# Kernel optimization log

Measured on AMD Instinct MI355X. Metric: run time of the kernel, lower is better.

## Reference

```python
import jax, jax.numpy as jnp
import numpy as np

NUM_NODES, NODE_F = 50000, 128
NUM_EDGES, EDGE_F = 500000, 128
B, N = 4096, 100
D = 64      # node_dim
T = 8       # time_dim
LN_EPS = 1e-5


def setup_inputs() -> dict:
    key = jax.random.key(0)
    ks = jax.random.split(key, 16)
    inp = {
        'src_neighbor_node_ids': jax.random.randint(ks[0], (B, N), 0, NUM_NODES),
        'src_neighbor_edge_ids': jax.random.randint(ks[1], (B, N), 0, NUM_EDGES),
        'src_neighbor_times': jax.random.uniform(ks[2], (B, N), dtype=jnp.float32),
        'dst_node_ids': jax.random.randint(ks[3], (B,), 0, NUM_NODES),
        'node_raw_features': jax.random.normal(ks[4], (NUM_NODES, NODE_F), jnp.float32),
        'edge_raw_features': jax.random.normal(ks[5], (NUM_EDGES, EDGE_F), jnp.float32),
        # projection layers (stored as [in, out])
        'W_feat': jax.random.normal(ks[6], (NODE_F, D), jnp.float32) / np.sqrt(NODE_F),
        'b_feat': jnp.zeros((D,), jnp.float32),
        'W_edge': jax.random.normal(ks[7], (1, D), jnp.float32),
        'b_edge': jnp.zeros((D,), jnp.float32),
        'W_time': jax.random.normal(ks[8], (T, D), jnp.float32) / np.sqrt(T),
        'b_time': jnp.zeros((D,), jnp.float32),
        'W_struct': jax.random.normal(ks[9], (1, D), jnp.float32),
        'b_struct': jnp.zeros((D,), jnp.float32),
        # time encoder (cosine basis with log-spaced frequencies)
        'w_tenc': (1.0 / 10 ** np.linspace(0, 9, T)).astype(np.float32),
        'b_tenc': jnp.zeros((T,), jnp.float32),
        # layernorm
        'ln_g': jnp.ones((D,), jnp.float32),
        'ln_b': jnp.zeros((D,), jnp.float32),
        # GCNConv
        'W_gcn': jax.random.normal(ks[10], (D, D), jnp.float32) / np.sqrt(D),
        'b_gcn': jnp.zeros((D,), jnp.float32),
        # output layer
        'W_out': jax.random.normal(ks[11], (D, D), jnp.float32) / np.sqrt(D),
        'b_out': jnp.zeros((D,), jnp.float32),
    }
    return inp


def reference(src_neighbor_node_ids, src_neighbor_edge_ids, src_neighbor_times,
              dst_node_ids, node_raw_features, edge_raw_features,
              W_feat, b_feat, W_edge, b_edge, W_time, b_time, W_struct, b_struct,
              w_tenc, b_tenc, ln_g, ln_b, W_gcn, b_gcn, W_out, b_out):
    f32 = jnp.float32
    nbr_raw = node_raw_features[src_neighbor_node_ids]            # [B,N,F]
    node_f = nbr_raw @ W_feat + b_feat                            # [B,N,D]
    edge_col = edge_raw_features[src_neighbor_edge_ids, 0][..., None]  # [B,N,1]
    edge_f = edge_col @ W_edge + b_edge
    t_enc = jnp.cos(src_neighbor_times[..., None] * w_tenc + b_tenc)   # [B,N,T]
    time_f = t_enc @ W_time + b_time
    co = (src_neighbor_node_ids == dst_node_ids[:, None]).astype(f32)[..., None]
    co_f = co @ W_struct + b_struct
    skill_nbr = nbr_raw[..., 0].astype(jnp.int32)                 # [B,N]
    skill_dst = node_raw_features[dst_node_ids, 0].astype(jnp.int32)  # [B]
    sim = (skill_nbr == skill_dst[:, None]).astype(f32)[..., None]
    sim_f = sim @ W_struct + b_struct
    fused = node_f + edge_f + time_f + co_f + sim_f               # [B,N,D]
    mu = fused.mean(-1, keepdims=True)
    var = ((fused - mu) ** 2).mean(-1, keepdims=True)
    fused = (fused - mu) * jax.lax.rsqrt(var + LN_EPS) * ln_g + ln_b
    # per-sample chain GCN: directed edges j -> j+1 for j in [0, v-2], v = #valid ids,
    # PyG gcn_norm with self loops: deg[j] = 1 + in_degree[j]
    h = fused @ W_gcn                                             # [B,N,D]
    v = (src_neighbor_node_ids > 0).sum(-1)                       # [B]
    pos = jnp.arange(N)[None, :]                                  # [1,N]
    has_in = ((pos >= 1) & (pos < v[:, None])).astype(f32)        # [B,N]
    deg = 1.0 + has_in
    dinv_sqrt = jax.lax.rsqrt(deg)
    h_prev = jnp.pad(h[:, :-1], ((0, 0), (1, 0), (0, 0)))
    d_prev = jnp.pad(dinv_sqrt[:, :-1], ((0, 0), (1, 0)))
    out = h / deg[..., None] + (has_in * d_prev * dinv_sqrt)[..., None] * h_prev + b_gcn
    gnn = jax.nn.relu(out)
    src_emb = gnn.mean(axis=1)                                    # [B,D] global_mean_pool over N
    dst_emb = node_raw_features[dst_node_ids] @ W_feat + b_feat
    src_emb = src_emb @ W_out + b_out
    dst_emb = dst_emb @ W_out + b_out
    return src_emb, dst_emb
```

## Files before the change

kernel.cpp:

```cpp
#include <hip/hip_runtime.h>
#include <stdint.h>

#define NUM_NODES 50000
#define B_ 4096
#define N_ 100

typedef float f32x4 __attribute__((ext_vector_type(4)));
typedef float f32x2 __attribute__((ext_vector_type(2)));
typedef int   i32x4 __attribute__((ext_vector_type(4)));
typedef short s16x8 __attribute__((ext_vector_type(8)));

__device__ inline unsigned short f2bf(float f) {
    unsigned u = __float_as_uint(f);
    u += 0x7fffu + ((u >> 16) & 1u);
    return (unsigned short)(u >> 16);
}

template <int CTRL>
__device__ inline float dpp_add(float x) {
    int t = __builtin_amdgcn_update_dpp(0, __float_as_int(x), CTRL, 0xf, 0xf, true);
    return x + __int_as_float(t);
}
__device__ inline float wave_sum64(float x) {
    x = dpp_add<0x111>(x);
    x = dpp_add<0x112>(x);
    x = dpp_add<0x114>(x);
    x = dpp_add<0x118>(x);
    x = dpp_add<0x142>(x);
    x = dpp_add<0x143>(x);
    return __int_as_float(__builtin_amdgcn_readlane(__float_as_int(x), 63));
}

__global__ __launch_bounds__(256) void k_pre(
    const float* __restrict__ node_raw, const float* __restrict__ W_feat,
    const float* __restrict__ b_feat, const float* __restrict__ W_gcn,
    const float* __restrict__ ln_g, const float* __restrict__ ln_b,
    const float* __restrict__ W_edge, const float* __restrict__ b_edge,
    const float* __restrict__ W_time, const float* __restrict__ b_time,
    const float* __restrict__ W_struct, const float* __restrict__ b_struct,
    float* __restrict__ proj, int* __restrict__ skill,
    float* __restrict__ hb, float* __restrict__ wmg, float* __restrict__ Mg,
    unsigned short* __restrict__ PGmF)
{
    __shared__ float red[4][64];
    __shared__ float PGms[12][64];
    __shared__ unsigned short WfB[16][64][8];
    int blk = blockIdx.x;
    int t = threadIdx.x;
    int dj = t & 63;

    if (blk == gridDim.x - 1) {
        int g = t >> 6;
        float acc = 0.f;
        #pragma unroll
        for (int i = 0; i < 16; ++i) {
            int dk = g * 16 + i;
            acc += ln_b[dk] * W_gcn[dk * 64 + dj];
        }
        red[g][dj] = acc;

        if (t < 64) {
            int d = t;
            float col[11];
            col[0] = W_edge[d];
            col[1] = W_struct[d];
            #pragma unroll
            for (int i = 0; i < 8; ++i) col[2 + i] = W_time[i * 64 + d];
            col[10] = b_edge[d] + b_time[d] + 2.f * b_struct[d];
            float wmv[11];
            #pragma unroll
            for (int j = 0; j < 11; ++j) wmv[j] = wave_sum64(col[j]) * (1.f / 64.f);
            float cc[11];
            #pragma unroll
            for (int j = 0; j < 11; ++j) cc[j] = col[j] - wmv[j];
            #pragma unroll
            for (int j = 0; j < 11; ++j) {
                #pragma unroll
                for (int k = j; k < 11; ++k) {
                    float m = wave_sum64(cc[j] * cc[k]);
                    if (t == 0) { Mg[j * 11 + k] = m; Mg[k * 11 + j] = m; }
                }
            }
            if (t == 0) {
                #pragma unroll
                for (int j = 0; j < 11; ++j) wmg[j] = wmv[j];
            }

            int j = t;
            float accp[12];
            #pragma unroll
            for (int m = 0; m < 12; ++m) accp[m] = 0.f;
            for (int d2 = 0; d2 < 64; ++d2) {
                float gg = ln_g[d2] * W_gcn[d2 * 64 + j];
                float bias_d = b_edge[d2] + b_time[d2] + 2.f * b_struct[d2];
                accp[0] = fmaf(W_edge[d2], gg, accp[0]);
                accp[1] = fmaf(W_struct[d2], gg, accp[1]);
                #pragma unroll
                for (int i = 0; i < 8; ++i)
                    accp[2 + i] = fmaf(W_time[i * 64 + d2], gg, accp[2 + i]);
                accp[10] = fmaf(bias_d, gg, accp[10]);
                accp[11] += gg;
            }
            #pragma unroll
            for (int m = 0; m < 12; ++m) PGms[m][j] = accp[m];
        }
        __syncthreads();
        if (g == 0) hb[dj] = red[0][dj] + red[1][dj] + red[2][dj] + red[3][dj];

        {
            int ct = t >> 6, l = t & 63;
            int col = ct * 16 + (l & 15);
            int ks = (l >> 4) * 8;
            s16x8 a2;
            #pragma unroll
            for (int j2 = 0; j2 < 8; ++j2) {
                int k = ks + j2;
                a2[j2] = (k < 12) ? (short)f2bf(PGms[k][col]) : (short)0;
            }
            *(s16x8*)(PGmF + ((size_t)ct * 64 + l) * 8) = a2;
        }
        return;
    }

    #pragma unroll
    for (int i = 0; i < 4; ++i) {
        int e = t + i * 256;
        int tile = e >> 6;
        int l = e & 63;
        int ct = tile >> 2, kt = tile & 3;
        int col = ct * 16 + (l & 15);
        int ks = kt * 32 + (l >> 4) * 8;
        s16x8 a;
        #pragma unroll
        for (int j = 0; j < 8; ++j)
            a[j] = (short)f2bf(W_feat[(ks + j) * 64 + col]);
        *(s16x8*)&WfB[tile][l][0] = a;
    }
    __syncthreads();

    int w = t >> 6, lane = t & 63;
    int rbase = blk * 64 + w * 16;
    int rA = rbase + (lane & 15);
    int rc = rA < NUM_NODES ? rA : (NUM_NODES - 1);
    int kq = lane >> 4;

    s16x8 A[4];
    float a0x = 0.f;
    #pragma unroll
    for (int kt = 0; kt < 4; ++kt) {
        const float* src = node_raw + (size_t)rc * 128 + kt * 32 + kq * 8;
        f32x4 v0 = *(const f32x4*)src;
        f32x4 v1 = *(const f32x4*)(src + 4);
        s16x8 a;
        a[0] = (short)f2bf(v0.x); a[1] = (short)f2bf(v0.y);
        a[2] = (short)f2bf(v0.z); a[3] = (short)f2bf(v0.w);
        a[4] = (short)f2bf(v1.x); a[5] = (short)f2bf(v1.y);
        a[6] = (short)f2bf(v1.z); a[7] = (short)f2bf(v1.w);
        A[kt] = a;
        if (kt == 0) a0x = v0.x;
    }
    if (kq == 0 && rA < NUM_NODES) skill[rA] = (int)a0x;

    f32x4 acc[4];
    #pragma unroll
    for (int ct = 0; ct < 4; ++ct) { f32x4 z = {0.f,0.f,0.f,0.f}; acc[ct] = z; }
    #pragma unroll
    for (int ct = 0; ct < 4; ++ct) {
        #pragma unroll
        for (int kt = 0; kt < 4; ++kt) {
            s16x8 bfr = *(const s16x8*)&WfB[ct * 4 + kt][lane][0];
            acc[ct] = __builtin_amdgcn_mfma_f32_16x16x32_bf16(A[kt], bfr, acc[ct], 0, 0, 0);
        }
    }
    #pragma unroll
    for (int ct = 0; ct < 4; ++ct) {
        int col = ct * 16 + (lane & 15);
        float bf = b_feat[col];
        #pragma unroll
        for (int j = 0; j < 4; ++j) {
            int row = rbase + kq * 4 + j;
            if (row < NUM_NODES)
                proj[(size_t)row * 64 + col] = acc[ct][j] + bf;
        }
    }
}

__global__ __launch_bounds__(256) void k_pg(
    const float* __restrict__ proj, const float* __restrict__ W_gcn,
    const float* __restrict__ ln_g,
    const float* __restrict__ W_out, const float* __restrict__ b_out,
    const float* __restrict__ W_edge, const float* __restrict__ b_edge,
    const float* __restrict__ W_time, const float* __restrict__ b_time,
    const float* __restrict__ W_struct, const float* __restrict__ b_struct,
    float* __restrict__ projG, float* __restrict__ dstE,
    float* __restrict__ stats)
{
    __shared__ unsigned short WgB[8][64][8];
    __shared__ unsigned short WoB[8][64][8];
    __shared__ unsigned short WsB[2][64][8];
    int t = threadIdx.x;

    #pragma unroll
    for (int i = 0; i < 2; ++i) {
        int e = t + i * 256;
        int tile = e >> 6, l = e & 63;
        int ct = tile >> 1, kt = tile & 1;
        int col = ct * 16 + (l & 15);
        int ks = kt * 32 + (l >> 4) * 8;
        s16x8 a, b2;
        #pragma unroll
        for (int j = 0; j < 8; ++j) {
            int k = ks + j;
            a[j]  = (short)f2bf(ln_g[k] * W_gcn[k * 64 + col]);
            b2[j] = (short)f2bf(W_out[k * 64 + col]);
        }
        *(s16x8*)&WgB[tile][l][0] = a;
        *(s16x8*)&WoB[tile][l][0] = b2;
    }
    if (t < 128) {
        int kt = t >> 6, l = t & 63;
        int col = l & 15;
        int ks = kt * 32 + (l >> 4) * 8;
        s16x8 a;
        #pragma unroll
        for (int j = 0; j < 8; ++j) {
            int d = ks + j;
            float v;
            if (col == 0) v = W_edge[d];
            else if (col == 1) v = W_struct[d];
            else if (col < 10) v = W_time[(col - 2) * 64 + d];
            else if (col == 10) v = b_edge[d] + b_time[d] + 2.f * b_struct[d];
            else if (col == 11) v = 1.f;
            else v = 0.f;
            a[j] = (short)f2bf(v);
        }
        *(s16x8*)&WsB[kt][l][0] = a;
    }
    __syncthreads();

    int w = t >> 6, lane = t & 63;
    int rbase = blockIdx.x * 64 + w * 16;
    int rA = rbase + (lane & 15);
    int rc = rA < NUM_NODES ? rA : (NUM_NODES - 1);
    int kq = lane >> 4;

    s16x8 Ahi[2], Alo[2], Qhi[2], Qlo[2];
    #pragma unroll
    for (int kt = 0; kt < 2; ++kt) {
        const float* src = proj + (size_t)rc * 64 + kt * 32 + kq * 8;
        f32x4 v0 = *(const f32x4*)src;
        f32x4 v1 = *(const f32x4*)(src + 4);
        #pragma unroll
        for (int j = 0; j < 8; ++j) {
            float v = (j < 4) ? v0[j] : v1[j - 4];
            unsigned short hi = f2bf(v);
            float rem = v - __uint_as_float((unsigned)hi << 16);
            Ahi[kt][j] = (short)hi;
            Alo[kt][j] = (short)f2bf(rem);
            float p2 = v * v;
            unsigned short h2 = f2bf(p2);
            float r2 = p2 - __uint_as_float((unsigned)h2 << 16);
            Qhi[kt][j] = (short)h2;
            Qlo[kt][j] = (short)f2bf(r2);
        }
    }

    f32x4 accG[4], accE[4];
    f32x4 accS = {0.f, 0.f, 0.f, 0.f}, accQ = {0.f, 0.f, 0.f, 0.f};
    #pragma unroll
    for (int ct = 0; ct < 4; ++ct) {
        f32x4 z = {0.f, 0.f, 0.f, 0.f};
        accG[ct] = z; accE[ct] = z;
    }
    #pragma unroll
    for (int ct = 0; ct < 4; ++ct) {
        #pragma unroll
        for (int kt = 0; kt < 2; ++kt) {
            s16x8 bg = *(const s16x8*)&WgB[ct * 2 + kt][lane][0];
            accG[ct] = __builtin_amdgcn_mfma_f32_16x16x32_bf16(Alo[kt], bg, accG[ct], 0, 0, 0);
            accG[ct] = __builtin_amdgcn_mfma_f32_16x16x32_bf16(Ahi[kt], bg, accG[ct], 0, 0, 0);
            s16x8 bo = *(const s16x8*)&WoB[ct * 2 + kt][lane][0];
            accE[ct] = __builtin_amdgcn_mfma_f32_16x16x32_bf16(Alo[kt], bo, accE[ct], 0, 0, 0);
            accE[ct] = __builtin_amdgcn_mfma_f32_16x16x32_bf16(Ahi[kt], bo, accE[ct], 0, 0, 0);
        }
    }
    #pragma unroll
    for (int kt = 0; kt < 2; ++kt) {
        s16x8 bs = *(const s16x8*)&WsB[kt][lane][0];
        accS = __builtin_amdgcn_mfma_f32_16x16x32_bf16(Alo[kt], bs, accS, 0, 0, 0);
        accS = __builtin_amdgcn_mfma_f32_16x16x32_bf16(Ahi[kt], bs, accS, 0, 0, 0);
        accQ = __builtin_amdgcn_mfma_f32_16x16x32_bf16(Qlo[kt], bs, accQ, 0, 0, 0);
        accQ = __builtin_amdgcn_mfma_f32_16x16x32_bf16(Qhi[kt], bs, accQ, 0, 0, 0);
    }

    #pragma unroll
    for (int ct = 0; ct < 4; ++ct) {
        int col = ct * 16 + (lane & 15);
        float bo_ = b_out[col];
        #pragma unroll
        for (int j = 0; j < 4; ++j) {
            int row = rbase + kq * 4 + j;
            if (row < NUM_NODES) {
                projG[(size_t)row * 64 + col] = accG[ct][j];
                dstE[(size_t)row * 64 + col] = accE[ct][j] + bo_;
            }
        }
    }
    int c = lane & 15;
    if (c <= 11) {
        #pragma unroll
        for (int j = 0; j < 4; ++j) {
            int row = rbase + kq * 4 + j;
            if (row < NUM_NODES) stats[(size_t)row * 16 + c] = accS[j];
        }
    }
    if (c == 11) {
        #pragma unroll
        for (int j = 0; j < 4; ++j) {
            int row = rbase + kq * 4 + j;
            if (row < NUM_NODES) stats[(size_t)row * 16 + 12] = accQ[j];
        }
    }
}

__global__ __launch_bounds__(256) void k_main(
    const int* __restrict__ ids, const int* __restrict__ eids,
    const float* __restrict__ times, const int* __restrict__ dst_ids,
    const float* __restrict__ edge_raw,
    const float* __restrict__ w_tenc, const float* __restrict__ b_tenc,
    const float* __restrict__ b_gcn, const float* __restrict__ W_out,
    const float* __restrict__ b_out,
    const float* __restrict__ projG, const float* __restrict__ dstE,
    const int* __restrict__ skill,
    const float* __restrict__ hb, const float* __restrict__ wmg,
    const float* __restrict__ Mg, const unsigned short* __restrict__ PGmF,
    const float* __restrict__ stats,
    float* __restrict__ out)
{
    __shared__ int ids_s[112];
    __shared__ unsigned short VA[112 * 32];
    __shared__ float rstd_s[112];
    __shared__ f32x2 cf_s[112];
    __shared__ float pooled[64];
    __shared__ int vcnt_w[4];

    int b = blockIdx.x;
    int t = threadIdx.x;
    int lane = t & 63, w = t >> 6;

    int dstb = dst_ids[b];
    int skdst = skill[dstb];

    int idx_c = t < N_ ? t : 0;
    int id_t = ids[b * N_ + idx_c];
    float tm_t = times[b * N_ + idx_c];
    int ei_t = eids[b * N_ + idx_c];
    if (t < 112) ids_s[t] = (t < N_) ? id_t : 0;
    unsigned long long bal = __ballot((t < N_) && (id_t > 0));
    if (lane == 0) vcnt_w[w] = __popcll(bal);
    float tc[8];
    #pragma unroll
    for (int i = 0; i < 8; ++i) tc[i] = __cosf(fmaf(tm_t, w_tenc[i], b_tenc[i]));
    __syncthreads();
    int v = vcnt_w[0] + vcnt_w[1] + vcnt_w[2] + vcnt_w[3];

    int colw = 16 * w + (lane & 15);
    int kq = lane >> 4;
    float pgv[7][4];
    #pragma unroll
    for (int mt = 0; mt < 7; ++mt) {
        i32x4 s4 = *(const i32x4*)&ids_s[mt * 16 + kq * 4];
        #pragma unroll
        for (int j = 0; j < 4; ++j)
            pgv[mt][j] = projG[(size_t)s4[j] * 64 + colw];
    }
    if (w == 3)
        out[(size_t)(B_ + b) * 64 + lane] = dstE[(size_t)dstb * 64 + lane];

    if (t < 112) {
        int n = t;
        bool hin = (n >= 1) && (n < v);
        float a_ = hin ? 0.5f : 1.f;
        float dprev = (n >= 2 && n <= v) ? 0.70710678118f : 1.f;
        float coef = hin ? dprev * 0.70710678118f : 0.f;
        f32x2 cf = {a_, coef};
        cf_s[t] = cf;
    }

    if (t < N_) {
        float e_t = edge_raw[(size_t)ei_t * 128];
        int sk_t = skill[id_t];
        const f32x4* sp4 = (const f32x4*)(stats + (size_t)id_t * 16);
        f32x4 s0 = sp4[0], s1 = sp4[1], s2 = sp4[2];
        float spp = stats[(size_t)id_t * 16 + 12];

        float u[11];
        u[0] = e_t;
        u[1] = (id_t == dstb ? 1.f : 0.f) + (sk_t == skdst ? 1.f : 0.f);
        #pragma unroll
        for (int i = 0; i < 8; ++i) u[2 + i] = tc[i];
        u[10] = 1.f;

        float pwv[11] = {s0.x, s0.y, s0.z, s0.w, s1.x, s1.y, s1.z, s1.w,
                         s2.x, s2.y, s2.z};
        float sp = s2.w;
        float dot_upw = 0.f, su_wm = 0.f;
        #pragma unroll
        for (int j = 0; j < 11; ++j) {
            dot_upw = fmaf(u[j], pwv[j], dot_upw);
            su_wm = fmaf(u[j], wmg[j], su_wm);
        }
        float mu = sp * (1.f / 64.f) + su_wm;
        float q = spp + sp * sp * (1.f / 64.f) + 2.f * dot_upw - 2.f * sp * mu;
        #pragma unroll
        for (int j = 0; j < 11; ++j) {
            float tj = 0.f;
            #pragma unroll
            for (int k = 0; k < 11; ++k) tj = fmaf(Mg[j * 11 + k], u[k], tj);
            q = fmaf(u[j], tj, q);
        }
        float rstd = rsqrtf(fmaxf(q, 0.f) * (1.f / 64.f) + 1e-5f);
        rstd_s[t] = rstd;

        unsigned short vv[32];
        #pragma unroll
        for (int j = 0; j < 11; ++j) vv[j] = f2bf(rstd * u[j]);
        vv[11] = f2bf(-rstd * mu);
        #pragma unroll
        for (int j = 12; j < 32; ++j) vv[j] = 0;
        #pragma unroll
        for (int c = 0; c < 4; ++c)
            *(s16x8*)((char*)VA + t * 64 + ((c ^ (t & 3)) * 16)) = *(const s16x8*)&vv[c * 8];
    } else if (t < 112) {
        rstd_s[t] = 0.f;
        s16x8 z = {0, 0, 0, 0, 0, 0, 0, 0};
        #pragma unroll
        for (int c = 0; c < 4; ++c)
            *(s16x8*)((char*)VA + t * 64 + c * 16) = z;
    }
    __syncthreads();

    s16x8 bfr = *(const s16x8*)(PGmF + ((size_t)w * 64 + lane) * 8);
    f32x4 acc[7];
    #pragma unroll
    for (int mt = 0; mt < 7; ++mt) {
        int row = mt * 16 + (lane & 15);
        s16x8 a = *(const s16x8*)((char*)VA + row * 64 + ((kq ^ (row & 3)) * 16));
        f32x4 z = {0.f, 0.f, 0.f, 0.f};
        acc[mt] = __builtin_amdgcn_mfma_f32_16x16x32_bf16(a, bfr, z, 0, 0, 0);
    }

    float hbv = hb[colw], bgc = b_gcn[colw];
    float carry = 0.f, po = 0.f;
    #pragma unroll
    for (int mt = 0; mt < 7; ++mt) {
        int nb = mt * 16 + kq * 4;
        f32x4 rs4 = *(const f32x4*)&rstd_s[nb];
        f32x4 cf01 = *(const f32x4*)&cf_s[nb];
        f32x4 cf23 = *(const f32x4*)&cf_s[nb + 2];
        float hh[4];
        #pragma unroll
        for (int j = 0; j < 4; ++j)
            hh[j] = fmaf(rs4[j], pgv[mt][j], acc[mt][j]) + hbv;

        float hup = __shfl_up(hh[3], 16, 64);
        float hpj = (kq > 0) ? hup : carry;

        float o0 = fmaf(hh[0], cf01.x, fmaf(cf01.y, hpj, bgc));
        float o1 = fmaf(hh[1], cf01.z, fmaf(cf01.w, hh[0], bgc));
        float o2 = fmaf(hh[2], cf23.x, fmaf(cf23.y, hh[1], bgc));
        float o3 = fmaf(hh[3], cf23.z, fmaf(cf23.w, hh[2], bgc));
        if (nb < N_)     po += fmaxf(o0, 0.f);
        if (nb + 1 < N_) po += fmaxf(o1, 0.f);
        if (nb + 2 < N_) po += fmaxf(o2, 0.f);
        if (nb + 3 < N_) po += fmaxf(o3, 0.f);

        carry = __shfl(hh[3], 48 + (lane & 15), 64);
    }
    po += __shfl_xor(po, 16, 64);
    po += __shfl_xor(po, 32, 64);
    if (lane < 16) pooled[colw] = po * (1.f / (float)N_);
    __syncthreads();

    if (w == 0) {
        float o = b_out[lane];
        #pragma unroll
        for (int dk4 = 0; dk4 < 16; ++dk4) {
            f32x4 p4 = *(const f32x4*)&pooled[dk4 * 4];
            o = fmaf(p4.x, W_out[(dk4 * 4 + 0) * 64 + lane], o);
            o = fmaf(p4.y, W_out[(dk4 * 4 + 1) * 64 + lane], o);
            o = fmaf(p4.z, W_out[(dk4 * 4 + 2) * 64 + lane], o);
            o = fmaf(p4.w, W_out[(dk4 * 4 + 3) * 64 + lane], o);
        }
        out[(size_t)b * 64 + lane] = o;
    }
}

extern "C" void kernel_launch(void* const* d_in, const int* in_sizes, int n_in,
                              void* d_out, int out_size, void* d_ws, size_t ws_size,
                              hipStream_t stream)
{
    const int*   ids      = (const int*)d_in[0];
    const int*   eids     = (const int*)d_in[1];
    const float* times    = (const float*)d_in[2];
    const int*   dst_ids  = (const int*)d_in[3];
    const float* node_raw = (const float*)d_in[4];
    const float* edge_raw = (const float*)d_in[5];
    const float* W_feat   = (const float*)d_in[6];
    const float* b_feat   = (const float*)d_in[7];
    const float* W_edge   = (const float*)d_in[8];
    const float* b_edge   = (const float*)d_in[9];
    const float* W_time   = (const float*)d_in[10];
    const float* b_time   = (const float*)d_in[11];
    const float* W_struct = (const float*)d_in[12];
    const float* b_struct = (const float*)d_in[13];
    const float* w_tenc   = (const float*)d_in[14];
    const float* b_tenc   = (const float*)d_in[15];
    const float* ln_g     = (const float*)d_in[16];
    const float* ln_b     = (const float*)d_in[17];
    const float* W_gcn    = (const float*)d_in[18];
    const float* b_gcn    = (const float*)d_in[19];
    const float* W_out    = (const float*)d_in[20];
    const float* b_out    = (const float*)d_in[21];

    char* ws = (char*)d_ws;
    float*          proj   = (float*)ws;
    int*            skill  = (int*)(ws + 12800000);
    float*          hb     = (float*)(ws + 13008192);
    float*          wmg    = (float*)(ws + 13008448);
    float*          Mg     = (float*)(ws + 13008512);
    unsigned short* PGmF   = (unsigned short*)(ws + 13009024);
    float*          stats  = (float*)(ws + 13100032);
    float*          projG  = (float*)(ws + 16400000);
    float*          dstE   = (float*)(ws + 29200000);

    k_pre<<<783, 256, 0, stream>>>(node_raw, W_feat, b_feat, W_gcn, ln_g, ln_b,
                                   W_edge, b_edge, W_time, b_time, W_struct, b_struct,
                                   proj, skill, hb, wmg, Mg, PGmF);
    k_pg<<<782, 256, 0, stream>>>(proj, W_gcn, ln_g, W_out, b_out,
                                  W_edge, b_edge, W_time, b_time, W_struct, b_struct,
                                  projG, dstE, stats);
    k_main<<<B_, 256, 0, stream>>>(ids, eids, times, dst_ids, edge_raw,
                                   w_tenc, b_tenc, b_gcn, W_out, b_out,
                                   projG, dstE, skill, hb, wmg, Mg, PGmF, stats,
                                   (float*)d_out);
}
```

Baseline: 70.41 us.

## Split k_main rows across two wave groups with 512-thread blocks

Doubles k_main's block size to 512 threads so the 7 row tiles are split between two groups of four waves (tiles 0-3 and 3-6, overlapping at tile 3 so the chain carry is correct), each owning a pooling range. The per-wave register array of projG gathers shrinks from 7 to 4 tiles, and a __syncthreads is removed by computing the valid count with per-wave ballots and recomputing GCN coefficients inline instead of staging them in shared memory. The goal is more latency hiding for the scattered projG gathers through higher occupancy. In exchange, one tile is computed twice, ids are reloaded from global memory per element, and a second pooled buffer must be summed.

```diff
diff --git a/kernel.cpp b/kernel.cpp
--- a/kernel.cpp
+++ b/kernel.cpp
@@ -323,7 +323,7 @@
     }
 }
 
-__global__ __launch_bounds__(256) void k_main(
+__global__ __launch_bounds__(512, 8) void k_main(
     const int* __restrict__ ids, const int* __restrict__ eids,
     const float* __restrict__ times, const int* __restrict__ dst_ids,
     const float* __restrict__ edge_raw,
@@ -337,57 +337,45 @@
     const float* __restrict__ stats,
     float* __restrict__ out)
 {
-    __shared__ int ids_s[112];
     __shared__ unsigned short VA[112 * 32];
     __shared__ float rstd_s[112];
-    __shared__ f32x2 cf_s[112];
-    __shared__ float pooled[64];
-    __shared__ int vcnt_w[4];
+    __shared__ float pooled[2][64];
 
     int b = blockIdx.x;
     int t = threadIdx.x;
     int lane = t & 63, w = t >> 6;
+    int cs = w & 3, rh = w >> 2;
 
     int dstb = dst_ids[b];
-    int skdst = skill[dstb];
-
-    int idx_c = t < N_ ? t : 0;
-    int id_t = ids[b * N_ + idx_c];
-    float tm_t = times[b * N_ + idx_c];
-    int ei_t = eids[b * N_ + idx_c];
-    if (t < 112) ids_s[t] = (t < N_) ? id_t : 0;
-    unsigned long long bal = __ballot((t < N_) && (id_t > 0));
-    if (lane == 0) vcnt_w[w] = __popcll(bal);
-    float tc[8];
-    #pragma unroll
-    for (int i = 0; i < 8; ++i) tc[i] = __cosf(fmaf(tm_t, w_tenc[i], b_tenc[i]));
-    __syncthreads();
-    int v = vcnt_w[0] + vcnt_w[1] + vcnt_w[2] + vcnt_w[3];
-
-    int colw = 16 * w + (lane & 15);
+
+    int idA = ids[b * N_ + lane];
+    int idB = ids[b * N_ + (lane < 36 ? 64 + lane : 0)];
+    unsigned long long balA = __ballot(idA > 0);
+    unsigned long long balB = __ballot((lane < 36) && (idB > 0));
+    int v = __popcll(balA) + __popcll(balB);
+
+    int colw = cs * 16 + (lane & 15);
     int kq = lane >> 4;
-    float pgv[7][4];
-    #pragma unroll
-    for (int mt = 0; mt < 7; ++mt) {
-        i32x4 s4 = *(const i32x4*)&ids_s[mt * 16 + kq * 4];
-        #pragma unroll
-        for (int j = 0; j < 4; ++j)
-            pgv[mt][j] = projG[(size_t)s4[j] * 64 + colw];
-    }
-    if (w == 3)
+    float pgv[4][4];
+    #pragma unroll
+    for (int mt = 0; mt < 4; ++mt) {
+        int gt = mt + rh * 3;
+        #pragma unroll
+        for (int j = 0; j < 4; ++j) {
+            int n = gt * 16 + kq * 4 + j;
+            int nc = n < N_ ? n : N_ - 1;
+            int idn = ids[b * N_ + nc];
+            pgv[mt][j] = projG[(size_t)idn * 64 + colw];
+        }
+    }
+    if (w == 7)
         out[(size_t)(B_ + b) * 64 + lane] = dstE[(size_t)dstb * 64 + lane];
 
-    if (t < 112) {
-        int n = t;
-        bool hin = (n >= 1) && (n < v);
-        float a_ = hin ? 0.5f : 1.f;
-        float dprev = (n >= 2 && n <= v) ? 0.70710678118f : 1.f;
-        float coef = hin ? dprev * 0.70710678118f : 0.f;
-        f32x2 cf = {a_, coef};
-        cf_s[t] = cf;
-    }
-
     if (t < N_) {
+        int skdst = skill[dstb];
+        int id_t = ids[b * N_ + t];
+        float tm_t = times[b * N_ + t];
+        int ei_t = eids[b * N_ + t];
         float e_t = edge_raw[(size_t)ei_t * 128];
         int sk_t = skill[id_t];
         const f32x4* sp4 = (const f32x4*)(stats + (size_t)id_t * 16);
@@ -398,7 +386,7 @@
         u[0] = e_t;
         u[1] = (id_t == dstb ? 1.f : 0.f) + (sk_t == skdst ? 1.f : 0.f);
         #pragma unroll
-        for (int i = 0; i < 8; ++i) u[2 + i] = tc[i];
+        for (int i = 0; i < 8; ++i) u[2 + i] = __cosf(fmaf(tm_t, w_tenc[i], b_tenc[i]));
         u[10] = 1.f;
 
         float pwv[11] = {s0.x, s0.y, s0.z, s0.w, s1.x, s1.y, s1.z, s1.w,
@@ -440,24 +428,24 @@
     }
     __syncthreads();
 
-    s16x8 bfr = *(const s16x8*)(PGmF + ((size_t)w * 64 + lane) * 8);
-    f32x4 acc[7];
-    #pragma unroll
-    for (int mt = 0; mt < 7; ++mt) {
-        int row = mt * 16 + (lane & 15);
+    s16x8 bfr = *(const s16x8*)(PGmF + ((size_t)cs * 64 + lane) * 8);
+    f32x4 acc[4];
+    #pragma unroll
+    for (int mt = 0; mt < 4; ++mt) {
+        int row = (mt + rh * 3) * 16 + (lane & 15);
         s16x8 a = *(const s16x8*)((char*)VA + row * 64 + ((kq ^ (row & 3)) * 16));
         f32x4 z = {0.f, 0.f, 0.f, 0.f};
         acc[mt] = __builtin_amdgcn_mfma_f32_16x16x32_bf16(a, bfr, z, 0, 0, 0);
     }
 
     float hbv = hb[colw], bgc = b_gcn[colw];
+    int plo = rh ? 64 : 0;
+    int phi = rh ? N_ : 64;
     float carry = 0.f, po = 0.f;
     #pragma unroll
-    for (int mt = 0; mt < 7; ++mt) {
-        int nb = mt * 16 + kq * 4;
+    for (int mt = 0; mt < 4; ++mt) {
+        int nb = (mt + rh * 3) * 16 + kq * 4;
         f32x4 rs4 = *(const f32x4*)&rstd_s[nb];
-        f32x4 cf01 = *(const f32x4*)&cf_s[nb];
-        f32x4 cf23 = *(const f32x4*)&cf_s[nb + 2];
         float hh[4];
         #pragma unroll
         for (int j = 0; j < 4; ++j)
@@ -465,32 +453,34 @@
 
         float hup = __shfl_up(hh[3], 16, 64);
         float hpj = (kq > 0) ? hup : carry;
-
-        float o0 = fmaf(hh[0], cf01.x, fmaf(cf01.y, hpj, bgc));
-        float o1 = fmaf(hh[1], cf01.z, fmaf(cf01.w, hh[0], bgc));
-        float o2 = fmaf(hh[2], cf23.x, fmaf(cf23.y, hh[1], bgc));
-        float o3 = fmaf(hh[3], cf23.z, fmaf(cf23.w, hh[2], bgc));
-        if (nb < N_)     po += fmaxf(o0, 0.f);
-        if (nb + 1 < N_) po += fmaxf(o1, 0.f);
-        if (nb + 2 < N_) po += fmaxf(o2, 0.f);
-        if (nb + 3 < N_) po += fmaxf(o3, 0.f);
-
+        #pragma unroll
+        for (int j = 0; j < 4; ++j) {
+            int n = nb + j;
+            bool hin = (n >= 1) && (n < v);
+            float a_ = hin ? 0.5f : 1.f;
+            float dprev = (n >= 2 && n <= v) ? 0.70710678118f : 1.f;
+            float coef = hin ? dprev * 0.70710678118f : 0.f;
+            float o = fmaf(hh[j], a_, fmaf(coef, hpj, bgc));
+            po += (n >= plo && n < phi) ? fmaxf(o, 0.f) : 0.f;
+            hpj = hh[j];
+        }
         carry = __shfl(hh[3], 48 + (lane & 15), 64);
     }
     po += __shfl_xor(po, 16, 64);
     po += __shfl_xor(po, 32, 64);
-    if (lane < 16) pooled[colw] = po * (1.f / (float)N_);
+    if (lane < 16) pooled[rh][colw] = po * (1.f / (float)N_);
     __syncthreads();
 
     if (w == 0) {
         float o = b_out[lane];
         #pragma unroll
         for (int dk4 = 0; dk4 < 16; ++dk4) {
-            f32x4 p4 = *(const f32x4*)&pooled[dk4 * 4];
-            o = fmaf(p4.x, W_out[(dk4 * 4 + 0) * 64 + lane], o);
-            o = fmaf(p4.y, W_out[(dk4 * 4 + 1) * 64 + lane], o);
-            o = fmaf(p4.z, W_out[(dk4 * 4 + 2) * 64 + lane], o);
-            o = fmaf(p4.w, W_out[(dk4 * 4 + 3) * 64 + lane], o);
+            f32x4 p0 = *(const f32x4*)&pooled[0][dk4 * 4];
+            f32x4 p1 = *(const f32x4*)&pooled[1][dk4 * 4];
+            o = fmaf(p0.x + p1.x, W_out[(dk4 * 4 + 0) * 64 + lane], o);
+            o = fmaf(p0.y + p1.y, W_out[(dk4 * 4 + 1) * 64 + lane], o);
+            o = fmaf(p0.z + p1.z, W_out[(dk4 * 4 + 2) * 64 + lane], o);
+            o = fmaf(p0.w + p1.w, W_out[(dk4 * 4 + 3) * 64 + lane], o);
         }
         out[(size_t)b * 64 + lane] = o;
     }
@@ -540,7 +530,7 @@
     k_pg<<<782, 256, 0, stream>>>(proj, W_gcn, ln_g, W_out, b_out,
                                   W_edge, b_edge, W_time, b_time, W_struct, b_struct,
                                   projG, dstE, stats);
-    k_main<<<B_, 256, 0, stream>>>(ids, eids, times, dst_ids, edge_raw,
+    k_main<<<B_, 512, 0, stream>>>(ids, eids, times, dst_ids, edge_raw,
                                    w_tenc, b_tenc, b_gcn, W_out, b_out,
                                    projG, dstE, skill, hb, wmg, Mg, PGmF, stats,
                                    (float*)d_out);
```

After: 81.62 us. 15.9% more time.
